# Performance work log

Hardware: AMD Instinct MI355X
Metric: run time of the kernel (lower is better)

Reference implementation:

```python
import jax, jax.numpy as jnp
import numpy as np

N = 100000
E = 1600000
IN_DIM, H1, H2, OUT_DIM = 32, 64, 64, 64
BETA = 0.2


def _glorot(key, shape):
    fan_in, fan_out = shape[0], shape[1]
    lim = float(np.sqrt(6.0 / (fan_in + fan_out)))
    return jax.random.uniform(key, shape, jnp.float32, -lim, lim)


def setup_inputs() -> dict:
    key = jax.random.key(0)
    ks = jax.random.split(key, 16)
    x = jax.random.normal(ks[0], (N, IN_DIM), jnp.float32)
    edge_index = jax.random.randint(ks[1], (2, E), 0, N, jnp.int64)
    impedance = jax.random.normal(ks[2], (N, 1), jnp.float32)
    return {
        "x": x,
        "edge_index": edge_index,
        "impedance": impedance,
        "W1": _glorot(ks[3], (IN_DIM, H1)), "b1": jnp.zeros((H1,), jnp.float32),
        "Wi1": _glorot(ks[4], (IN_DIM, H1)),
        "W2": _glorot(ks[5], (H1, H2)), "b2": jnp.zeros((H2,), jnp.float32),
        "Wi2": _glorot(ks[6], (H1, H2)),
        "W3": _glorot(ks[7], (H2, OUT_DIM)), "b3": jnp.zeros((OUT_DIM,), jnp.float32),
        "Wi3": _glorot(ks[8], (H2, OUT_DIM)),
        "Wfc": _glorot(ks[9], (H2, 1)), "bfc": jnp.zeros((1,), jnp.float32),
    }


def _conv(x, row, col, impedance, Wl, bl, Wi):
    # dense transforms (per-node)
    out = x @ Wl + bl                 # [N, C]
    imp_mod = x @ Wi                  # [N, C]
    # per-edge message: x_j (source=row) + impedance[row] * imp_mod[col]
    msg = out[row] + impedance[row] * imp_mod[col]   # [E, C]
    # scatter-add into target nodes (col), aggr='add'
    return jax.ops.segment_sum(msg, col, num_segments=N)


def reference(x, edge_index, impedance, W1, b1, Wi1, W2, b2, Wi2, W3, b3, Wi3, Wfc, bfc):
    row, col = edge_index[0], edge_index[1]
    h = _conv(x, row, col, impedance, W1, b1, Wi1)
    h = jnp.where(h >= 0, h, BETA * h)  # leaky_relu(negative_slope=beta)
    h = _conv(h, row, col, impedance, W2, b2, Wi2)
    h = jnp.where(h >= 0, h, BETA * h)
    h = _conv(h, row, col, impedance, W3, b3, Wi3)
    return h @ Wfc + bfc              # [N, 1]
```

## Files before the change

### kernel.cpp

```cpp
#include <hip/hip_runtime.h>


#define BINW    128
#define CHUNK   4096
#define BINFIX  3072

typedef __attribute__((ext_vector_type(8))) short bf16x8;
typedef __attribute__((ext_vector_type(4))) float f32x4;

__device__ inline unsigned short f2bf(float f) {
    unsigned u = __float_as_uint(f);
    unsigned r = u + 0x7fffu + ((u >> 16) & 1u);
    return (unsigned short)(r >> 16);
}
__device__ inline float bflo(unsigned u) { return __uint_as_float(u << 16); }
__device__ inline float bfhi(unsigned u) { return __uint_as_float(u & 0xffff0000u); }

__global__ __launch_bounds__(256) void bin_scatter_fix(const int* __restrict__ row,
        const int* __restrict__ col, int* __restrict__ cursor,
        int* __restrict__ binBuf, int E, int nbin) {
    __shared__ int      wpackl[CHUNK];
    __shared__ unsigned short wbin[CHUNK];
    __shared__ int      hist[1024];
    __shared__ int      basel[1024];

    int e0 = blockIdx.x * CHUNK;
    int cnt = E - e0; if (cnt > CHUNK) cnt = CHUNK;
    if (cnt <= 0) return;
    int tid = threadIdx.x;

    for (int b = tid; b < nbin; b += 256) hist[b] = 0;
    for (int i = tid; i < cnt; i += 256) {
        int r = row[e0 + i], v = col[e0 + i];
        wpackl[i] = (r << 7) | (v & (BINW - 1));
        wbin[i]  = (unsigned short)(v >> 7);
    }
    __syncthreads();
    for (int i = tid; i < cnt; i += 256) atomicAdd(&hist[wbin[i]], 1);
    __syncthreads();
    for (int b = tid; b < nbin; b += 256) {
        int h = hist[b];
        basel[b] = h ? atomicAdd(&cursor[b], h) : 0;
        hist[b] = 0;
    }
    __syncthreads();
    for (int i = tid; i < cnt; i += 256) {
        int b = wbin[i];
        int off = basel[b] + atomicAdd(&hist[b], 1);
        if (off < BINFIX)
            binBuf[(size_t)b * BINFIX + off] = wpackl[i];
    }
}

__global__ __launch_bounds__(256) void bin_phaseB2(const int* __restrict__ cursor,
        const int* __restrict__ binBuf, const float* __restrict__ imp,
        int* __restrict__ rows, int2* __restrict__ ptr2, float* __restrict__ S,
        int* __restrict__ gcur, int n) {
    __shared__ int   dhist[BINW];
    __shared__ int   dpre[BINW];
    __shared__ int   doff[BINW];
    __shared__ float dS[BINW];
    __shared__ int   dstb_s;

    int b = blockIdx.x;
    int srcb = b * BINFIX;
    int cnt = cursor[b]; if (cnt > BINFIX) cnt = BINFIX;
    int tid = threadIdx.x;
    int v0 = b << 7;

    if (tid < BINW) { dhist[tid] = 0; doff[tid] = 0; dS[tid] = 0.f; }
    __syncthreads();
    for (int i = tid; i < cnt; i += 256)
        atomicAdd(&dhist[binBuf[srcb + i] & (BINW - 1)], 1);
    __syncthreads();
    if (tid < BINW) dpre[tid] = dhist[tid];
    __syncthreads();
    for (int d = 1; d < BINW; d <<= 1) {
        int v = 0;
        if (tid < BINW) v = dpre[tid] + ((tid >= d) ? dpre[tid - d] : 0);
        __syncthreads();
        if (tid < BINW) dpre[tid] = v;
        __syncthreads();
    }
    if (tid == 0) dstb_s = atomicAdd(gcur, cnt);
    __syncthreads();
    int dstb = dstb_s;
    if (tid < BINW) {
        int v = v0 + tid;
        if (v < n) {
            int s = dstb + dpre[tid] - dhist[tid];
            ptr2[v] = make_int2(s, s + dhist[tid]);
        }
    }
    for (int i = tid; i < cnt; i += 256) {
        int w = binBuf[srcb + i];
        int j = w & (BINW - 1);
        int r = w >> 7;
        int pos = dstb + dpre[j] - dhist[j] + atomicAdd(&doff[j], 1);
        rows[pos] = r;
        atomicAdd(&dS[j], imp[r]);
    }
    __syncthreads();
    if (tid < BINW) {
        int v = v0 + tid;
        if (v < n) S[v] = dS[tid];
    }
}

__global__ __launch_bounds__(256) void wpack_all(
        const float* __restrict__ W1, const float* __restrict__ Wi1,
        const float* __restrict__ W2, const float* __restrict__ Wi2,
        const float* __restrict__ W3, const float* __restrict__ Wi3,
        const float* __restrict__ b3, const float* __restrict__ Wfc,
        unsigned short* __restrict__ wf1, unsigned short* __restrict__ wf2,
        float* __restrict__ wfc3) {
    int blk = blockIdx.x;
    int tid = threadIdx.x;
    if (blk == 2) {
        if (tid < 128) {
            int k = tid & 63;
            const float* src = (tid < 64) ? W3 : Wi3;
            float s = 0.f;
            for (int c = 0; c < 64; ++c) s = fmaf(src[k * 64 + c], Wfc[c], s);
            wfc3[tid] = s;
        }
        if (tid == 128) {
            float bb = 0.f;
            for (int c = 0; c < 64; ++c) bb = fmaf(b3[c], Wfc[c], bb);
            wfc3[128] = bb;
        }
        return;
    }
    const float *W, *Wi; unsigned short* dst; int KC;
    if (blk == 0) { W = W1; Wi = Wi1; dst = wf1; KC = 1; }
    else          { W = W2; Wi = Wi2; dst = wf2; KC = 2; }
    int SLOTS = 2 * KC * 4 * 64;
    for (int s = tid; s < SLOTS; s += 256) {
        int l  = s & 63;
        int ct = (s >> 6) & 3;
        int kc = (s >> 8) % KC;
        int m  = s / (256 * KC);
        int k   = kc * 32 + ((l >> 4) << 3);
        int c   = ct * 16 + (l & 15);
        const float* src = m ? Wi : W;
        unsigned short t[8];
#pragma unroll
        for (int e = 0; e < 8; ++e) t[e] = f2bf(src[(k + e) * 64 + c]);
        *(uint4*)(dst + (size_t)s * 8) = make_uint4(
            (unsigned)t[0] | ((unsigned)t[1] << 16),
            (unsigned)t[2] | ((unsigned)t[3] << 16),
            (unsigned)t[4] | ((unsigned)t[5] << 16),
            (unsigned)t[6] | ((unsigned)t[7] << 16));
    }
}

template<int K, bool FP32IN>
__global__ __launch_bounds__(256) void gemm_mfma(
        const void* __restrict__ inp, const unsigned short* __restrict__ wf,
        const float* __restrict__ bias, const float* __restrict__ S,
        unsigned short* __restrict__ outb, unsigned short* __restrict__ imb, int n) {
    constexpr int KC = K / 32;
    int lane = threadIdx.x & 63;
    int node0 = blockIdx.x * 64 + (threadIdx.x >> 6) * 16;
    if (node0 >= n) return;

    int arow = node0 + (lane & 15);
    if (arow >= n) arow = n - 1;
    int koff = (lane >> 4) << 3;

    f32x4 z = {0.f, 0.f, 0.f, 0.f};
    f32x4 accW[4] = {z, z, z, z};
    f32x4 accI[4] = {z, z, z, z};

#pragma unroll
    for (int kc = 0; kc < KC; ++kc) {
        bf16x8 a;
        if (FP32IN) {
            const float* ap = (const float*)inp + (size_t)arow * K + koff + kc * 32;
            float4 f0 = *(const float4*)ap;
            float4 f1 = *(const float4*)(ap + 4);
            unsigned short t[8] = { f2bf(f0.x), f2bf(f0.y), f2bf(f0.z), f2bf(f0.w),
                                    f2bf(f1.x), f2bf(f1.y), f2bf(f1.z), f2bf(f1.w) };
            a = *(const bf16x8*)t;
        } else {
            const unsigned short* ap = (const unsigned short*)inp + (size_t)arow * K + koff + kc * 32;
            a = *(const bf16x8*)ap;
        }
#pragma unroll
        for (int ct = 0; ct < 4; ++ct) {
            bf16x8 bw = *(const bf16x8*)(wf + ((((size_t)0 * KC + kc) * 4 + ct) * 64 + lane) * 8);
            bf16x8 bi = *(const bf16x8*)(wf + ((((size_t)1 * KC + kc) * 4 + ct) * 64 + lane) * 8);
            accW[ct] = __builtin_amdgcn_mfma_f32_16x16x32_bf16(a, bw, accW[ct], 0, 0, 0);
            accI[ct] = __builtin_amdgcn_mfma_f32_16x16x32_bf16(a, bi, accI[ct], 0, 0, 0);
        }
    }

    int colb = lane & 15;
    int rbase = node0 + ((lane >> 4) << 2);
    float sv[4];
#pragma unroll
    for (int j = 0; j < 4; ++j) {
        int r = rbase + j;
        sv[j] = (r < n) ? S[r] : 0.f;
    }
#pragma unroll
    for (int ct = 0; ct < 4; ++ct) {
        int c = ct * 16 + colb;
        float bb = bias[c];
#pragma unroll
        for (int j = 0; j < 4; ++j) {
            int r = rbase + j;
            if (r < n) {
                outb[(size_t)r * 64 + c] = f2bf(accW[ct][j] + bb);
                imb [(size_t)r * 64 + c] = f2bf(sv[j] * accI[ct][j]);
            }
        }
    }
}

#define G8_BODY(rX) { \
        uint4 a = *(const uint4*)(outb + (size_t)(rX) * 64 + sub * 8); \
        acc[0] += bflo(a.x); acc[1] += bfhi(a.x); \
        acc[2] += bflo(a.y); acc[3] += bfhi(a.y); \
        acc[4] += bflo(a.z); acc[5] += bfhi(a.z); \
        acc[6] += bflo(a.w); acc[7] += bfhi(a.w); }

__device__ inline void gather_core(const int* __restrict__ rows,
        const unsigned short* __restrict__ outb,
        const unsigned short* __restrict__ imb, int v, int sub, float* acc,
        int p0, int p1) {
    const unsigned short* ip = imb + (size_t)v * 64 + sub * 8;
    uint4 i0 = *(const uint4*)ip;
    acc[0] = bflo(i0.x); acc[1] = bfhi(i0.x);
    acc[2] = bflo(i0.y); acc[3] = bfhi(i0.y);
    acc[4] = bflo(i0.z); acc[5] = bfhi(i0.z);
    acc[6] = bflo(i0.w); acc[7] = bfhi(i0.w);

    int i = p0;
    for (; i + 8 <= p1; i += 8) {
        int r0 = rows[i],     r1 = rows[i + 1], r2 = rows[i + 2], r3 = rows[i + 3];
        int r4 = rows[i + 4], r5 = rows[i + 5], r6 = rows[i + 6], r7 = rows[i + 7];
        uint4 a0 = *(const uint4*)(outb + (size_t)r0 * 64 + sub * 8);
        uint4 a1 = *(const uint4*)(outb + (size_t)r1 * 64 + sub * 8);
        uint4 a2 = *(const uint4*)(outb + (size_t)r2 * 64 + sub * 8);
        uint4 a3 = *(const uint4*)(outb + (size_t)r3 * 64 + sub * 8);
        uint4 a4 = *(const uint4*)(outb + (size_t)r4 * 64 + sub * 8);
        uint4 a5 = *(const uint4*)(outb + (size_t)r5 * 64 + sub * 8);
        uint4 a6 = *(const uint4*)(outb + (size_t)r6 * 64 + sub * 8);
        uint4 a7 = *(const uint4*)(outb + (size_t)r7 * 64 + sub * 8);
        acc[0] += (bflo(a0.x) + bflo(a1.x)) + (bflo(a2.x) + bflo(a3.x))
                + (bflo(a4.x) + bflo(a5.x)) + (bflo(a6.x) + bflo(a7.x));
        acc[1] += (bfhi(a0.x) + bfhi(a1.x)) + (bfhi(a2.x) + bfhi(a3.x))
                + (bfhi(a4.x) + bfhi(a5.x)) + (bfhi(a6.x) + bfhi(a7.x));
        acc[2] += (bflo(a0.y) + bflo(a1.y)) + (bflo(a2.y) + bflo(a3.y))
                + (bflo(a4.y) + bflo(a5.y)) + (bflo(a6.y) + bflo(a7.y));
        acc[3] += (bfhi(a0.y) + bfhi(a1.y)) + (bfhi(a2.y) + bfhi(a3.y))
                + (bfhi(a4.y) + bfhi(a5.y)) + (bfhi(a6.y) + bfhi(a7.y));
        acc[4] += (bflo(a0.z) + bflo(a1.z)) + (bflo(a2.z) + bflo(a3.z))
                + (bflo(a4.z) + bflo(a5.z)) + (bflo(a6.z) + bflo(a7.z));
        acc[5] += (bfhi(a0.z) + bfhi(a1.z)) + (bfhi(a2.z) + bfhi(a3.z))
                + (bfhi(a4.z) + bfhi(a5.z)) + (bfhi(a6.z) + bfhi(a7.z));
        acc[6] += (bflo(a0.w) + bflo(a1.w)) + (bflo(a2.w) + bflo(a3.w))
                + (bflo(a4.w) + bflo(a5.w)) + (bflo(a6.w) + bflo(a7.w));
        acc[7] += (bfhi(a0.w) + bfhi(a1.w)) + (bfhi(a2.w) + bfhi(a3.w))
                + (bfhi(a4.w) + bfhi(a5.w)) + (bfhi(a6.w) + bfhi(a7.w));
    }
    for (; i + 4 <= p1; i += 4) {
        int r0 = rows[i], r1 = rows[i + 1], r2 = rows[i + 2], r3 = rows[i + 3];
        uint4 a0 = *(const uint4*)(outb + (size_t)r0 * 64 + sub * 8);
        uint4 a1 = *(const uint4*)(outb + (size_t)r1 * 64 + sub * 8);
        uint4 a2 = *(const uint4*)(outb + (size_t)r2 * 64 + sub * 8);
        uint4 a3 = *(const uint4*)(outb + (size_t)r3 * 64 + sub * 8);
        acc[0] += bflo(a0.x) + bflo(a1.x) + bflo(a2.x) + bflo(a3.x);
        acc[1] += bfhi(a0.x) + bfhi(a1.x) + bfhi(a2.x) + bfhi(a3.x);
        acc[2] += bflo(a0.y) + bflo(a1.y) + bflo(a2.y) + bflo(a3.y);
        acc[3] += bfhi(a0.y) + bfhi(a1.y) + bfhi(a2.y) + bfhi(a3.y);
        acc[4] += bflo(a0.z) + bflo(a1.z) + bflo(a2.z) + bflo(a3.z);
        acc[5] += bfhi(a0.z) + bfhi(a1.z) + bfhi(a2.z) + bfhi(a3.z);
        acc[6] += bflo(a0.w) + bflo(a1.w) + bflo(a2.w) + bflo(a3.w);
        acc[7] += bfhi(a0.w) + bfhi(a1.w) + bfhi(a2.w) + bfhi(a3.w);
    }
    for (; i < p1; ++i) G8_BODY(rows[i]);
}

__global__ __launch_bounds__(256) void gather_hb(const int2* __restrict__ ptr2,
        const int* __restrict__ rows, const unsigned short* __restrict__ outb,
        const unsigned short* __restrict__ imb, unsigned short* __restrict__ hb, int n) {
    int t = threadIdx.x;
    int v = blockIdx.x * 32 + (t >> 3);
    if (v >= n) return;
    int sub = t & 7;
    int2 p = ptr2[v];
    float acc[8];
    gather_core(rows, outb, imb, v, sub, acc, p.x, p.y);
    unsigned w[4];
#pragma unroll
    for (int q = 0; q < 4; ++q) {
        float v0 = acc[2 * q], v1 = acc[2 * q + 1];
        v0 = (v0 >= 0.f) ? v0 : 0.2f * v0;
        v1 = (v1 >= 0.f) ? v1 : 0.2f * v1;
        w[q] = (unsigned)f2bf(v0) | ((unsigned)f2bf(v1) << 16);
    }
    *(uint4*)(hb + (size_t)v * 64 + sub * 8) = make_uint4(w[0], w[1], w[2], w[3]);
}

__global__ __launch_bounds__(256) void gather_g(const int2* __restrict__ ptr2,
        const int* __restrict__ rows, const unsigned short* __restrict__ outb,
        const unsigned short* __restrict__ imb, const float* __restrict__ S,
        const float* __restrict__ wfc3, const float* __restrict__ bfc,
        float* __restrict__ g, float* __restrict__ gio, int n) {
    int t = threadIdx.x;
    int v = blockIdx.x * 32 + (t >> 3);
    if (v >= n) return;
    int sub = t & 7;
    int2 p = ptr2[v];
    float acc[8];
    gather_core(rows, outb, imb, v, sub, acc, p.x, p.y);

    float dg = 0.f, di = 0.f;
#pragma unroll
    for (int j = 0; j < 8; ++j) {
        float h = acc[j];
        h = (h >= 0.f) ? h : 0.2f * h;
        dg = fmaf(h, wfc3[sub * 8 + j], dg);
        di = fmaf(h, wfc3[64 + sub * 8 + j], di);
    }
    dg += __shfl_down(dg, 4, 8);
    dg += __shfl_down(dg, 2, 8);
    dg += __shfl_down(dg, 1, 8);
    di += __shfl_down(di, 4, 8);
    di += __shfl_down(di, 2, 8);
    di += __shfl_down(di, 1, 8);
    if (sub == 0) {
        g[v]   = dg;
        gio[v] = bfc[0] + (float)(p.y - p.x) * wfc3[128] + S[v] * di;
    }
}

__global__ __launch_bounds__(256) void gather_sc(const int2* __restrict__ ptr2,
        const int* __restrict__ rows, const float* __restrict__ g,
        const float* __restrict__ gio, float* __restrict__ o, int n) {
    int t = threadIdx.x;
    int v = blockIdx.x * 64 + (t >> 2);
    if (v >= n) return;
    int j = t & 3;
    int2 p = ptr2[v];
    float s = 0.f;
    for (int i = p.x + j; i < p.y; i += 4) s += g[rows[i]];
    s += __shfl_down(s, 2, 4);
    s += __shfl_down(s, 1, 4);
    if (j == 0) o[v] = gio[v] + s;
}

extern "C" void kernel_launch(void* const* d_in, const int* in_sizes, int n_in,
                              void* d_out, int out_size, void* d_ws, size_t ws_size,
                              hipStream_t stream) {
    const float* x   = (const float*)d_in[0];
    const int*   ei  = (const int*)d_in[1];
    const float* imp = (const float*)d_in[2];
    const float* W1  = (const float*)d_in[3];
    const float* b1  = (const float*)d_in[4];
    const float* Wi1 = (const float*)d_in[5];
    const float* W2  = (const float*)d_in[6];
    const float* b2  = (const float*)d_in[7];
    const float* Wi2 = (const float*)d_in[8];
    const float* W3  = (const float*)d_in[9];
    const float* b3  = (const float*)d_in[10];
    const float* Wi3 = (const float*)d_in[11];
    const float* Wfc = (const float*)d_in[12];
    const float* bfc = (const float*)d_in[13];

    int n = in_sizes[0] / 32;
    int E = in_sizes[1] / 2;
    const int* row = ei;
    const int* col = ei + E;
    int nbin = (n + BINW - 1) / BINW;

    size_t off = 0;
    auto alloc = [&](size_t words) {
        size_t cur = off;
        off += (words + 15) & ~(size_t)15;
        return cur;
    };
    int* wsw = (int*)d_ws;
    float*          S        = (float*)(wsw + alloc(n));
    int2*           ptr2     = (int2*)(wsw + alloc((size_t)n * 2));
    int*            cursor   = wsw + alloc(1024);
    int*            gcur     = wsw + alloc(16);
    int*            binBuf   = wsw + alloc((size_t)nbin * BINFIX);
    int*            rowsA    = wsw + alloc(E);
    unsigned short* outb     = (unsigned short*)(wsw + alloc((size_t)n * 32));
    unsigned short* imb      = (unsigned short*)(wsw + alloc((size_t)n * 32));
    unsigned short* hb       = (unsigned short*)(wsw + alloc((size_t)n * 32));
    float*          g        = (float*)(wsw + alloc(n));
    float*          gio      = (float*)(wsw + alloc(n));
    unsigned short* wf1      = (unsigned short*)(wsw + alloc(2048));
    unsigned short* wf2      = (unsigned short*)(wsw + alloc(4096));
    float*          wfc3     = (float*)(wsw + alloc(144));

    int gA = (E + CHUNK - 1) / CHUNK;

    hipMemsetAsync(cursor, 0, (1024 + 16) * sizeof(int), stream);
    bin_scatter_fix<<<gA, 256, 0, stream>>>(row, col, cursor, binBuf, E, nbin);
    bin_phaseB2   <<<nbin, 256, 0, stream>>>(cursor, binBuf, imp, rowsA, ptr2, S, gcur, n);

    wpack_all<<<3, 256, 0, stream>>>(W1, Wi1, W2, Wi2, W3, Wi3, b3, Wfc, wf1, wf2, wfc3);

    int gm = (n + 63) / 64;
    int gg = (n + 31) / 32;
    int gs = (n + 63) / 64;

    gemm_mfma<32, true><<<gm, 256, 0, stream>>>(x, wf1, b1, S, outb, imb, n);
    gather_hb<<<gg, 256, 0, stream>>>(ptr2, rowsA, outb, imb, hb, n);

    gemm_mfma<64, false><<<gm, 256, 0, stream>>>(hb, wf2, b2, S, outb, imb, n);
    gather_g<<<gg, 256, 0, stream>>>(ptr2, rowsA, outb, imb, S, wfc3, bfc, g, gio, n);

    gather_sc<<<gs, 256, 0, stream>>>(ptr2, rowsA, g, gio, (float*)d_out, n);
}
```

Measured before the change: 202.3 us.

## Fuse edge binning with layer-1 GEMM and defer S scaling to gather

Merges the edge-binning scatter kernel and the first-layer MFMA GEMM into one launch: blocks below gA do the binning and the rest run the GEMM. This removes the first GEMM's dependence on S, which is instead applied as a scale factor inside gather_hb. The chunk size is doubled with 512-thread blocks. bin_phaseB2 now stages the bin in LDS and uses four replicated S accumulators to cut atomic contention. The intent is fewer launches and overlap of independent work, at the cost of much larger LDS use in the fused kernel and a different bf16 rounding point for the impedance product.

```diff
diff --git a/kernel.cpp b/kernel.cpp
--- a/kernel.cpp
+++ b/kernel.cpp
@@ -2,7 +2,7 @@
 
 
 #define BINW    128
-#define CHUNK   4096
+#define CHUNK   8192
 #define BINFIX  3072
 
 typedef __attribute__((ext_vector_type(8))) short bf16x8;
@@ -15,97 +15,6 @@
 }
 __device__ inline float bflo(unsigned u) { return __uint_as_float(u << 16); }
 __device__ inline float bfhi(unsigned u) { return __uint_as_float(u & 0xffff0000u); }
-
-__global__ __launch_bounds__(256) void bin_scatter_fix(const int* __restrict__ row,
-        const int* __restrict__ col, int* __restrict__ cursor,
-        int* __restrict__ binBuf, int E, int nbin) {
-    __shared__ int      wpackl[CHUNK];
-    __shared__ unsigned short wbin[CHUNK];
-    __shared__ int      hist[1024];
-    __shared__ int      basel[1024];
-
-    int e0 = blockIdx.x * CHUNK;
-    int cnt = E - e0; if (cnt > CHUNK) cnt = CHUNK;
-    if (cnt <= 0) return;
-    int tid = threadIdx.x;
-
-    for (int b = tid; b < nbin; b += 256) hist[b] = 0;
-    for (int i = tid; i < cnt; i += 256) {
-        int r = row[e0 + i], v = col[e0 + i];
-        wpackl[i] = (r << 7) | (v & (BINW - 1));
-        wbin[i]  = (unsigned short)(v >> 7);
-    }
-    __syncthreads();
-    for (int i = tid; i < cnt; i += 256) atomicAdd(&hist[wbin[i]], 1);
-    __syncthreads();
-    for (int b = tid; b < nbin; b += 256) {
-        int h = hist[b];
-        basel[b] = h ? atomicAdd(&cursor[b], h) : 0;
-        hist[b] = 0;
-    }
-    __syncthreads();
-    for (int i = tid; i < cnt; i += 256) {
-        int b = wbin[i];
-        int off = basel[b] + atomicAdd(&hist[b], 1);
-        if (off < BINFIX)
-            binBuf[(size_t)b * BINFIX + off] = wpackl[i];
-    }
-}
-
-__global__ __launch_bounds__(256) void bin_phaseB2(const int* __restrict__ cursor,
-        const int* __restrict__ binBuf, const float* __restrict__ imp,
-        int* __restrict__ rows, int2* __restrict__ ptr2, float* __restrict__ S,
-        int* __restrict__ gcur, int n) {
-    __shared__ int   dhist[BINW];
-    __shared__ int   dpre[BINW];
-    __shared__ int   doff[BINW];
-    __shared__ float dS[BINW];
-    __shared__ int   dstb_s;
-
-    int b = blockIdx.x;
-    int srcb = b * BINFIX;
-    int cnt = cursor[b]; if (cnt > BINFIX) cnt = BINFIX;
-    int tid = threadIdx.x;
-    int v0 = b << 7;
-
-    if (tid < BINW) { dhist[tid] = 0; doff[tid] = 0; dS[tid] = 0.f; }
-    __syncthreads();
-    for (int i = tid; i < cnt; i += 256)
-        atomicAdd(&dhist[binBuf[srcb + i] & (BINW - 1)], 1);
-    __syncthreads();
-    if (tid < BINW) dpre[tid] = dhist[tid];
-    __syncthreads();
-    for (int d = 1; d < BINW; d <<= 1) {
-        int v = 0;
-        if (tid < BINW) v = dpre[tid] + ((tid >= d) ? dpre[tid - d] : 0);
-        __syncthreads();
-        if (tid < BINW) dpre[tid] = v;
-        __syncthreads();
-    }
-    if (tid == 0) dstb_s = atomicAdd(gcur, cnt);
-    __syncthreads();
-    int dstb = dstb_s;
-    if (tid < BINW) {
-        int v = v0 + tid;
-        if (v < n) {
-            int s = dstb + dpre[tid] - dhist[tid];
-            ptr2[v] = make_int2(s, s + dhist[tid]);
-        }
-    }
-    for (int i = tid; i < cnt; i += 256) {
-        int w = binBuf[srcb + i];
-        int j = w & (BINW - 1);
-        int r = w >> 7;
-        int pos = dstb + dpre[j] - dhist[j] + atomicAdd(&doff[j], 1);
-        rows[pos] = r;
-        atomicAdd(&dS[j], imp[r]);
-    }
-    __syncthreads();
-    if (tid < BINW) {
-        int v = v0 + tid;
-        if (v < n) S[v] = dS[tid];
-    }
-}
 
 __global__ __launch_bounds__(256) void wpack_all(
         const float* __restrict__ W1, const float* __restrict__ Wi1,
@@ -154,16 +63,13 @@
     }
 }
 
-template<int K, bool FP32IN>
-__global__ __launch_bounds__(256) void gemm_mfma(
-        const void* __restrict__ inp, const unsigned short* __restrict__ wf,
-        const float* __restrict__ bias, const float* __restrict__ S,
-        unsigned short* __restrict__ outb, unsigned short* __restrict__ imb, int n) {
+template<int K, bool FP32IN, bool MULS>
+__device__ inline void gemm_body(const void* __restrict__ inp,
+        const unsigned short* __restrict__ wf, const float* __restrict__ bias,
+        const float* __restrict__ S, unsigned short* __restrict__ outb,
+        unsigned short* __restrict__ imb, int n, int node0, int lane) {
     constexpr int KC = K / 32;
-    int lane = threadIdx.x & 63;
-    int node0 = blockIdx.x * 64 + (threadIdx.x >> 6) * 16;
     if (node0 >= n) return;
-
     int arow = node0 + (lane & 15);
     if (arow >= n) arow = n - 1;
     int koff = (lane >> 4) << 3;
@@ -201,7 +107,7 @@
 #pragma unroll
     for (int j = 0; j < 4; ++j) {
         int r = rbase + j;
-        sv[j] = (r < n) ? S[r] : 0.f;
+        sv[j] = MULS ? ((r < n) ? S[r] : 0.f) : 1.f;
     }
 #pragma unroll
     for (int ct = 0; ct < 4; ++ct) {
@@ -212,10 +118,124 @@
             int r = rbase + j;
             if (r < n) {
                 outb[(size_t)r * 64 + c] = f2bf(accW[ct][j] + bb);
-                imb [(size_t)r * 64 + c] = f2bf(sv[j] * accI[ct][j]);
+                imb [(size_t)r * 64 + c] = f2bf(MULS ? (sv[j] * accI[ct][j]) : accI[ct][j]);
             }
         }
     }
+}
+
+__global__ __launch_bounds__(512) void mega1(
+        const int* __restrict__ row, const int* __restrict__ col,
+        int* __restrict__ cursor, int* __restrict__ binBuf, int E, int nbin, int gA,
+        const float* __restrict__ x, const unsigned short* __restrict__ wf1,
+        const float* __restrict__ b1, unsigned short* __restrict__ outb,
+        unsigned short* __restrict__ imb, int n) {
+    __shared__ int      wpackl[CHUNK];
+    __shared__ unsigned short wbin[CHUNK];
+    __shared__ int      hist[1024];
+    __shared__ int      basel[1024];
+
+    int bid = blockIdx.x;
+    int tid = threadIdx.x;
+
+    if (bid < gA) {
+        int e0 = bid * CHUNK;
+        int cnt = E - e0; if (cnt > CHUNK) cnt = CHUNK;
+        if (cnt <= 0) return;
+        for (int b = tid; b < nbin; b += 512) hist[b] = 0;
+        for (int i = tid; i < cnt; i += 512) {
+            int r = row[e0 + i], v = col[e0 + i];
+            wpackl[i] = (r << 7) | (v & (BINW - 1));
+            wbin[i]  = (unsigned short)(v >> 7);
+        }
+        __syncthreads();
+        for (int i = tid; i < cnt; i += 512) atomicAdd(&hist[wbin[i]], 1);
+        __syncthreads();
+        for (int b = tid; b < nbin; b += 512) {
+            int h = hist[b];
+            basel[b] = h ? atomicAdd(&cursor[b], h) : 0;
+            hist[b] = 0;
+        }
+        __syncthreads();
+        for (int i = tid; i < cnt; i += 512) {
+            int b = wbin[i];
+            int off = basel[b] + atomicAdd(&hist[b], 1);
+            if (off < BINFIX)
+                binBuf[(size_t)b * BINFIX + off] = wpackl[i];
+        }
+    } else {
+        int node0 = (bid - gA) * 128 + (tid >> 6) * 16;
+        gemm_body<32, true, false>(x, wf1, b1, nullptr, outb, imb, n, node0, tid & 63);
+    }
+}
+
+__global__ __launch_bounds__(256) void bin_phaseB2(const int* __restrict__ cursor,
+        const int* __restrict__ binBuf, const float* __restrict__ imp,
+        int* __restrict__ rows, int2* __restrict__ ptr2, float* __restrict__ S,
+        int* __restrict__ gcur, int n) {
+    __shared__ int   ein[BINFIX];
+    __shared__ int   dhist[BINW];
+    __shared__ int   dpre[BINW];
+    __shared__ int   doff[BINW];
+    __shared__ float dS[4][BINW];
+    __shared__ int   dstb_s;
+
+    int b = blockIdx.x;
+    int srcb = b * BINFIX;
+    int cnt = cursor[b]; if (cnt > BINFIX) cnt = BINFIX;
+    int tid = threadIdx.x;
+    int v0 = b << 7;
+
+    if (tid < BINW) {
+        dhist[tid] = 0; doff[tid] = 0;
+        dS[0][tid] = 0.f; dS[1][tid] = 0.f; dS[2][tid] = 0.f; dS[3][tid] = 0.f;
+    }
+    for (int i = tid; i < cnt; i += 256) ein[i] = binBuf[srcb + i];
+    __syncthreads();
+    for (int i = tid; i < cnt; i += 256) atomicAdd(&dhist[ein[i] & (BINW - 1)], 1);
+    __syncthreads();
+    if (tid < BINW) dpre[tid] = dhist[tid];
+    __syncthreads();
+    for (int d = 1; d < BINW; d <<= 1) {
+        int v = 0;
+        if (tid < BINW) v = dpre[tid] + ((tid >= d) ? dpre[tid - d] : 0);
+        __syncthreads();
+        if (tid < BINW) dpre[tid] = v;
+        __syncthreads();
+    }
+    if (tid == 0) dstb_s = atomicAdd(gcur, cnt);
+    __syncthreads();
+    int dstb = dstb_s;
+    if (tid < BINW) {
+        int v = v0 + tid;
+        if (v < n) {
+            int s = dstb + dpre[tid] - dhist[tid];
+            ptr2[v] = make_int2(s, s + dhist[tid]);
+        }
+    }
+    int rep = tid & 3;
+    for (int i = tid; i < cnt; i += 256) {
+        int w = ein[i];
+        int j = w & (BINW - 1);
+        int r = w >> 7;
+        int pos = dstb + dpre[j] - dhist[j] + atomicAdd(&doff[j], 1);
+        rows[pos] = r;
+        atomicAdd(&dS[rep][j], imp[r]);
+    }
+    __syncthreads();
+    if (tid < BINW) {
+        int v = v0 + tid;
+        if (v < n) S[v] = (dS[0][tid] + dS[1][tid]) + (dS[2][tid] + dS[3][tid]);
+    }
+}
+
+template<int K>
+__global__ __launch_bounds__(256) void gemm_mfma2(
+        const unsigned short* __restrict__ inp, const unsigned short* __restrict__ wf,
+        const float* __restrict__ bias, const float* __restrict__ S,
+        unsigned short* __restrict__ outb, unsigned short* __restrict__ imb, int n) {
+    int node0 = blockIdx.x * 64 + (threadIdx.x >> 6) * 16;
+    gemm_body<K, false, true>(inp, wf, bias, S, outb, imb, n, node0, threadIdx.x & 63);
 }
 
 #define G8_BODY(rX) { \
@@ -228,13 +248,13 @@
 __device__ inline void gather_core(const int* __restrict__ rows,
         const unsigned short* __restrict__ outb,
         const unsigned short* __restrict__ imb, int v, int sub, float* acc,
-        int p0, int p1) {
+        int p0, int p1, float scale) {
     const unsigned short* ip = imb + (size_t)v * 64 + sub * 8;
     uint4 i0 = *(const uint4*)ip;
-    acc[0] = bflo(i0.x); acc[1] = bfhi(i0.x);
-    acc[2] = bflo(i0.y); acc[3] = bfhi(i0.y);
-    acc[4] = bflo(i0.z); acc[5] = bfhi(i0.z);
-    acc[6] = bflo(i0.w); acc[7] = bfhi(i0.w);
+    acc[0] = scale * bflo(i0.x); acc[1] = scale * bfhi(i0.x);
+    acc[2] = scale * bflo(i0.y); acc[3] = scale * bfhi(i0.y);
+    acc[4] = scale * bflo(i0.z); acc[5] = scale * bfhi(i0.z);
+    acc[6] = scale * bflo(i0.w); acc[7] = scale * bfhi(i0.w);
 
     int i = p0;
     for (; i + 8 <= p1; i += 8) {
@@ -285,14 +305,15 @@
 
 __global__ __launch_bounds__(256) void gather_hb(const int2* __restrict__ ptr2,
         const int* __restrict__ rows, const unsigned short* __restrict__ outb,
-        const unsigned short* __restrict__ imb, unsigned short* __restrict__ hb, int n) {
+        const unsigned short* __restrict__ imb, const float* __restrict__ S,
+        unsigned short* __restrict__ hb, int n) {
     int t = threadIdx.x;
     int v = blockIdx.x * 32 + (t >> 3);
     if (v >= n) return;
     int sub = t & 7;
     int2 p = ptr2[v];
     float acc[8];
-    gather_core(rows, outb, imb, v, sub, acc, p.x, p.y);
+    gather_core(rows, outb, imb, v, sub, acc, p.x, p.y, S[v]);
     unsigned w[4];
 #pragma unroll
     for (int q = 0; q < 4; ++q) {
@@ -315,7 +336,7 @@
     int sub = t & 7;
     int2 p = ptr2[v];
     float acc[8];
-    gather_core(rows, outb, imb, v, sub, acc, p.x, p.y);
+    gather_core(rows, outb, imb, v, sub, acc, p.x, p.y, 1.f);
 
     float dg = 0.f, di = 0.f;
 #pragma unroll
@@ -398,22 +419,25 @@
     unsigned short* wf2      = (unsigned short*)(wsw + alloc(4096));
     float*          wfc3     = (float*)(wsw + alloc(144));
 
-    int gA = (E + CHUNK - 1) / CHUNK;
+    int gA  = (E + CHUNK - 1) / CHUNK;
+    int gm1 = (n + 127) / 128;
 
     hipMemsetAsync(cursor, 0, (1024 + 16) * sizeof(int), stream);
-    bin_scatter_fix<<<gA, 256, 0, stream>>>(row, col, cursor, binBuf, E, nbin);
-    bin_phaseB2   <<<nbin, 256, 0, stream>>>(cursor, binBuf, imp, rowsA, ptr2, S, gcur, n);
 
     wpack_all<<<3, 256, 0, stream>>>(W1, Wi1, W2, Wi2, W3, Wi3, b3, Wfc, wf1, wf2, wfc3);
+
+    mega1<<<gA + gm1, 512, 0, stream>>>(row, col, cursor, binBuf, E, nbin, gA,
+            x, wf1, b1, outb, imb, n);
+
+    bin_phaseB2<<<nbin, 256, 0, stream>>>(cursor, binBuf, imp, rowsA, ptr2, S, gcur, n);
 
     int gm = (n + 63) / 64;
     int gg = (n + 31) / 32;
     int gs = (n + 63) / 64;
 
-    gemm_mfma<32, true><<<gm, 256, 0, stream>>>(x, wf1, b1, S, outb, imb, n);
-    gather_hb<<<gg, 256, 0, stream>>>(ptr2, rowsA, outb, imb, hb, n);
-
-    gemm_mfma<64, false><<<gm, 256, 0, stream>>>(hb, wf2, b2, S, outb, imb, n);
+    gather_hb<<<gg, 256, 0, stream>>>(ptr2, rowsA, outb, imb, S, hb, n);
+
+    gemm_mfma2<64><<<gm, 256, 0, stream>>>(hb, wf2, b2, S, outb, imb, n);
     gather_g<<<gg, 256, 0, stream>>>(ptr2, rowsA, outb, imb, S, wfc3, bfc, g, gio, n);
 
     gather_sc<<<gs, 256, 0, stream>>>(ptr2, rowsA, g, gio, (float*)d_out, n);
```

After: 189.3 us (median of 2 runs). -6.4%, faster.
